# Optimization experiments

Hardware: AMD Instinct MI355X
Metric: run time of the kernel (lower is better)

The kernel has to match this reference:

```python
import jax, jax.numpy as jnp
import numpy as np


def setup_inputs() -> dict:
    key = jax.random.key(0)
    ks = jax.random.split(key, 13)
    B, T, F = 4096, 512, 64
    P, M = 64, 64  # price / metrics embedding dims
    TD, ED = 1, 8  # target_dim, explanatory_dim
    s = 0.05
    return {
        "input_seq": jax.random.normal(ks[0], (B, T, F), jnp.float32),
        "m_Wih": jax.random.normal(ks[1], (M, F + P), jnp.float32) * s,
        "m_Whh": jax.random.normal(ks[2], (M, M), jnp.float32) * s,
        "m_bih": jax.random.normal(ks[3], (M,), jnp.float32) * s,
        "m_bhh": jax.random.normal(ks[4], (M,), jnp.float32) * s,
        "p_Wih": jax.random.normal(ks[5], (P, F + M), jnp.float32) * s,
        "p_Whh": jax.random.normal(ks[6], (P, P), jnp.float32) * s,
        "p_bih": jax.random.normal(ks[7], (P,), jnp.float32) * s,
        "p_bhh": jax.random.normal(ks[8], (P,), jnp.float32) * s,
        "price_lin_W": jax.random.normal(ks[9], (TD, P), jnp.float32) * s,
        "price_lin_b": jax.random.normal(ks[10], (TD,), jnp.float32) * s,
        "metrics_lin_W": jax.random.normal(ks[11], (ED, M), jnp.float32) * s,
        "metrics_lin_b": jax.random.normal(ks[12], (ED,), jnp.float32) * s,
    }


def reference(input_seq, m_Wih, m_Whh, m_bih, m_bhh,
              p_Wih, p_Whh, p_bih, p_bhh,
              price_lin_W, price_lin_b, metrics_lin_W, metrics_lin_b):
    B = input_seq.shape[0]
    P = p_Whh.shape[0]
    M = m_Whh.shape[0]
    p0 = jnp.zeros((B, P), input_seq.dtype)
    m0 = jnp.zeros((B, M), input_seq.dtype)

    def step(carry, x_t):  # x_t: [B, F]
        p, m = carry
        # metrics cell: input = cat(x_t, price_embedding)
        m = jnp.tanh(jnp.concatenate([x_t, p], axis=1) @ m_Wih.T + m_bih
                     + m @ m_Whh.T + m_bhh)
        # price cell: input = cat(x_t, metrics_embedding)
        p = jnp.tanh(jnp.concatenate([x_t, m], axis=1) @ p_Wih.T + p_bih
                     + p @ p_Whh.T + p_bhh)
        return (p, m), None

    (p, m), _ = jax.lax.scan(step, (p0, m0), jnp.swapaxes(input_seq, 0, 1))
    # dropout in eval mode = identity
    price_pred = p @ price_lin_W.T + price_lin_b
    metrics_pred = m @ metrics_lin_W.T + metrics_lin_b
    return (price_pred, metrics_pred)
```

## Files before the change

kernel.cpp:

```cpp
#include <hip/hip_runtime.h>

typedef short bf16x8 __attribute__((ext_vector_type(8)));
typedef float f32x4 __attribute__((ext_vector_type(4)));
typedef int   int4v  __attribute__((ext_vector_type(4)));

#define MFMA16(a, b, c) __builtin_amdgcn_mfma_f32_16x16x32_bf16((a), (b), (c), 0, 0, 0)

static constexpr int T_LEN = 512;
static constexpr int F_DIM = 64;
static constexpr int NB    = 8;
static constexpr float C1  = 2.885390081777927f;

__device__ __forceinline__ unsigned short brne(float f) {
  unsigned u = __float_as_uint(f);
  return (unsigned short)((u + 0x7fffu + ((u >> 16) & 1u)) >> 16);
}

__device__ __forceinline__ int cvtpk(float lo, float hi) {
  int r;
  asm("v_cvt_pk_bf16_f32 %0, %1, %2" : "=v"(r) : "v"(lo), "v"(hi));
  return r;
}

__device__ __forceinline__ bf16x8 cvt8(const float4 &a, const float4 &b) {
  int4v d = {cvtpk(a.x, a.y), cvtpk(a.z, a.w), cvtpk(b.x, b.y), cvtpk(b.z, b.w)};
  union { int4v i; bf16x8 h; } u;
  u.i = d;
  return u.h;
}

__device__ __forceinline__ void swap32(float &a, float &b) {
  auto r = __builtin_amdgcn_permlane32_swap(__float_as_int(a), __float_as_int(b),
                                            false, false);
  a = __int_as_float(r[0]);
  b = __int_as_float(r[1]);
}

__device__ __forceinline__ float xor1(float v) {
  return __int_as_float(__builtin_amdgcn_mov_dpp(__float_as_int(v), 0xB1, 0xF, 0xF, true));
}

__device__ __forceinline__ float tanh_fold(float s, float c2) {
  float e  = __builtin_amdgcn_exp2f(__builtin_fmaf(s, C1, c2));
  float rc = __builtin_amdgcn_rcpf(e + 1.0f);
  return __builtin_fmaf(-2.0f, rc, 1.0f);
}

template<int PAR, bool FIN>
__device__ __forceinline__ void epilogue(
    const f32x4 &a0, const f32x4 &a1, float c2,
    unsigned short (*buf)[72], float (*fin)[68],
    int wofs, bool evn, int rowA, int j)
{
  float z0 = a0[0] + a1[0];
  float z1 = a0[1] + a1[1];
  float z2 = a0[2] + a1[2];
  float z3 = a0[3] + a1[3];
  swap32(z0, z2);
  swap32(z1, z3);
  float sA = (PAR == 0) ? z0 : z2;
  float sB = (PAR == 0) ? z1 : z3;
  float tA = tanh_fold(sA, c2);
  float tB = tanh_fold(sB, c2);
  float nA = xor1(tA);
  float nB = xor1(tB);
  if (evn) {
    unsigned short *p = &buf[0][0];
    *(unsigned *)(p + wofs)      = (unsigned)cvtpk(tA, nA);
    *(unsigned *)(p + wofs + 72) = (unsigned)cvtpk(tB, nB);
  }
  if (FIN) {
    fin[rowA][j]     = tA;
    fin[rowA + 1][j] = tB;
  }
}

template<int PAR, bool FIN>
__device__ __forceinline__ void step_cells(
    int arow, int g8, int j, int wofs, bool evn, int rowA,
    const bf16x8 &x0, const bf16x8 &x1,
    const bf16x8 (&Bm)[6], const bf16x8 (&Bp)[6],
    float c2m, float c2p, const f32x4 &Z,
    unsigned short (*sm_c)[72], unsigned short (*sm_p)[72],
    unsigned short (*sp_c)[72], unsigned short (*sp_p)[72],
    float (*mfin)[68], float (*pfin)[68])
{
  bf16x8 p0 = *(const bf16x8 *)&sp_p[arow][g8];
  bf16x8 p1 = *(const bf16x8 *)&sp_p[arow][32 + g8];

  {
    bf16x8 m0 = *(const bf16x8 *)&sm_p[arow][g8];
    bf16x8 m1 = *(const bf16x8 *)&sm_p[arow][32 + g8];
    f32x4 a0 = MFMA16(x0, Bm[0], Z);
    f32x4 a1 = MFMA16(x1, Bm[1], Z);
    a0 = MFMA16(p0, Bm[2], a0);
    a1 = MFMA16(p1, Bm[3], a1);
    a0 = MFMA16(m0, Bm[4], a0);
    a1 = MFMA16(m1, Bm[5], a1);
    epilogue<PAR, FIN>(a0, a1, c2m, sm_c, mfin, wofs, evn, rowA, j);
  }
  __syncthreads();
  {
    bf16x8 n0 = *(const bf16x8 *)&sm_c[arow][g8];
    bf16x8 n1 = *(const bf16x8 *)&sm_c[arow][32 + g8];
    f32x4 a0 = MFMA16(x0, Bp[0], Z);
    f32x4 a1 = MFMA16(x1, Bp[1], Z);
    a0 = MFMA16(n0, Bp[2], a0);
    a1 = MFMA16(n1, Bp[3], a1);
    a0 = MFMA16(p0, Bp[4], a0);
    a1 = MFMA16(p1, Bp[5], a1);
    epilogue<PAR, FIN>(a0, a1, c2p, sp_c, pfin, wofs, evn, rowA, j);
  }
  __syncthreads();
}

__global__ __launch_bounds__(256, 2)
void mr_rnn_kernel(const float *__restrict__ x,
                   const float *__restrict__ mWih, const float *__restrict__ mWhh,
                   const float *__restrict__ mbih, const float *__restrict__ mbhh,
                   const float *__restrict__ pWih, const float *__restrict__ pWhh,
                   const float *__restrict__ pbih, const float *__restrict__ pbhh,
                   const float *__restrict__ plW,  const float *__restrict__ plb,
                   const float *__restrict__ mlW,  const float *__restrict__ mlb,
                   float *__restrict__ out, int B)
{
  __shared__ __align__(16) unsigned short sm[2][NB][72], sp[2][NB][72];
  __shared__ __align__(16) float s_mfin[NB][68], s_pfin[NB][68];

  const int tid  = threadIdx.x;
  const int lane = tid & 63;
  const int q    = tid >> 6;
  const int l15  = lane & 15;
  const int arow = l15 & (NB - 1);
  const int half = l15 >> 3;
  const int g    = lane >> 4;
  const int j    = q * 16 + l15;
  const int b0   = blockIdx.x * NB;
  const int g8   = g * 8;
  const int rowA = ((lane & 16) >> 2) | ((lane >> 5) << 1);
  const bool evn = (l15 & 1) == 0;
  const int wofs = rowA * 72 + (j & ~1);

  bf16x8 Bm[6], Bp[6];
#pragma unroll
  for (int kt = 0; kt < 6; ++kt) {
    const int k0 = kt * 32 + g8;
#pragma unroll
    for (int i = 0; i < 8; ++i) {
      const int k = k0 + i;
      float wm = (k < 128) ? mWih[j * 128 + k] : mWhh[j * 64 + (k - 128)];
      float wp = (k < 128) ? pWih[j * 128 + k] : pWhh[j * 64 + (k - 128)];
      Bm[kt][i] = (short)brne(wm);
      Bp[kt][i] = (short)brne(wp);
    }
  }
  const float c2m = C1 * (mbih[j] + mbhh[j]);
  const float c2p = C1 * (pbih[j] + pbhh[j]);
  const f32x4 Z = {0.f, 0.f, 0.f, 0.f};

  for (int idx = tid; idx < NB * 72; idx += 256) {
    const int bb = idx / 72, kk = idx % 72;
    sm[1][bb][kk] = 0;
    sp[1][bb][kk] = 0;
  }

  const float *pxl = x + ((size_t)(b0 + arow) * T_LEN + half) * F_DIM + g8;
  float4 A0 = *(const float4 *)(pxl);
  float4 A1 = *(const float4 *)(pxl + 4);
  float4 A2 = *(const float4 *)(pxl + 32);
  float4 A3 = *(const float4 *)(pxl + 36);
  bf16x8 x0 = cvt8(A0, A1);
  bf16x8 x1 = cvt8(A2, A3);
  __syncthreads();

#pragma unroll 1
  for (int t = 0; t < T_LEN - 2; t += 2) {
    pxl += 2 * F_DIM;
    A0 = *(const float4 *)(pxl);
    A1 = *(const float4 *)(pxl + 4);
    A2 = *(const float4 *)(pxl + 32);
    A3 = *(const float4 *)(pxl + 36);
    step_cells<0, false>(arow, g8, j, wofs, evn, rowA, x0, x1, Bm, Bp, c2m, c2p, Z,
                         sm[0], sm[1], sp[0], sp[1], s_mfin, s_pfin);
    step_cells<1, false>(arow, g8, j, wofs, evn, rowA, x0, x1, Bm, Bp, c2m, c2p, Z,
                         sm[1], sm[0], sp[1], sp[0], s_mfin, s_pfin);
    x0 = cvt8(A0, A1);
    x1 = cvt8(A2, A3);
  }
  step_cells<0, false>(arow, g8, j, wofs, evn, rowA, x0, x1, Bm, Bp, c2m, c2p, Z,
                       sm[0], sm[1], sp[0], sp[1], s_mfin, s_pfin);
  step_cells<1, true>(arow, g8, j, wofs, evn, rowA, x0, x1, Bm, Bp, c2m, c2p, Z,
                      sm[1], sm[0], sp[1], sp[0], s_mfin, s_pfin);

  if (tid < NB) {
    const int b = tid;
    float acc = plb[0];
#pragma unroll 1
    for (int k = 0; k < 64; ++k) acc += s_pfin[b][k] * plW[k];
    out[b0 + b] = acc;
  } else if (tid < NB + NB * 8) {
    const int r = tid - NB;
    const int b = r >> 3, e = r & 7;
    float acc = mlb[e];
#pragma unroll 1
    for (int k = 0; k < 64; ++k) acc += s_mfin[b][k] * mlW[e * 64 + k];
    out[(size_t)B + (size_t)(b0 + b) * 8 + e] = acc;
  }
}

extern "C" void kernel_launch(void* const* d_in, const int* in_sizes, int n_in,
                              void* d_out, int out_size, void* d_ws, size_t ws_size,
                              hipStream_t stream) {
  (void)n_in; (void)out_size; (void)d_ws; (void)ws_size;
  const float* x    = (const float*)d_in[0];
  const float* mWih = (const float*)d_in[1];
  const float* mWhh = (const float*)d_in[2];
  const float* mbih = (const float*)d_in[3];
  const float* mbhh = (const float*)d_in[4];
  const float* pWih = (const float*)d_in[5];
  const float* pWhh = (const float*)d_in[6];
  const float* pbih = (const float*)d_in[7];
  const float* pbhh = (const float*)d_in[8];
  const float* plW  = (const float*)d_in[9];
  const float* plb  = (const float*)d_in[10];
  const float* mlW  = (const float*)d_in[11];
  const float* mlb  = (const float*)d_in[12];
  const int B = in_sizes[0] / (T_LEN * F_DIM);
  const int nblk = B / NB;
  mr_rnn_kernel<<<dim3(nblk), dim3(256), 0, stream>>>(
      x, mWih, mWhh, mbih, mbhh, pWih, pWhh, pbih, pbhh,
      plW, plb, mlW, mlb, (float*)d_out, B);
}
```

Baseline: 287.0 us.

## Halve batch per block to 4 rows and use 2 waves each owning 32 outputs

Each block now handles 4 batch rows with 128 threads (2 waves) instead of 8 rows with 4 waves. Each wave computes two 16-column output tiles with interleaved MFMA chains, and the result redistribution uses permlane16/permlane32 swaps. The goal is twice as many blocks for better CU coverage and cheaper barriers with fewer waves. In exchange each wave holds twice the weight registers and does twice the MFMA work per step, which lengthens the serial per-step latency.

```diff
diff --git a/kernel.cpp b/kernel.cpp
--- a/kernel.cpp
+++ b/kernel.cpp
@@ -2,13 +2,12 @@
 
 typedef short bf16x8 __attribute__((ext_vector_type(8)));
 typedef float f32x4 __attribute__((ext_vector_type(4)));
-typedef int   int4v  __attribute__((ext_vector_type(4)));
 
 #define MFMA16(a, b, c) __builtin_amdgcn_mfma_f32_16x16x32_bf16((a), (b), (c), 0, 0, 0)
 
 static constexpr int T_LEN = 512;
 static constexpr int F_DIM = 64;
-static constexpr int NB    = 8;
+static constexpr int NB    = 4;
 static constexpr float C1  = 2.885390081777927f;
 
 __device__ __forceinline__ unsigned short brne(float f) {
@@ -23,19 +22,13 @@
 }
 
 __device__ __forceinline__ bf16x8 cvt8(const float4 &a, const float4 &b) {
+  typedef int int4v __attribute__((ext_vector_type(4)));
   int4v d = {cvtpk(a.x, a.y), cvtpk(a.z, a.w), cvtpk(b.x, b.y), cvtpk(b.z, b.w)};
   union { int4v i; bf16x8 h; } u;
   u.i = d;
   return u.h;
 }
 
-__device__ __forceinline__ void swap32(float &a, float &b) {
-  auto r = __builtin_amdgcn_permlane32_swap(__float_as_int(a), __float_as_int(b),
-                                            false, false);
-  a = __int_as_float(r[0]);
-  b = __int_as_float(r[1]);
-}
-
 __device__ __forceinline__ float xor1(float v) {
   return __int_as_float(__builtin_amdgcn_mov_dpp(__float_as_int(v), 0xB1, 0xF, 0xF, true));
 }
@@ -46,41 +39,26 @@
   return __builtin_fmaf(-2.0f, rc, 1.0f);
 }
 
-template<int PAR, bool FIN>
-__device__ __forceinline__ void epilogue(
-    const f32x4 &a0, const f32x4 &a1, float c2,
-    unsigned short (*buf)[72], float (*fin)[68],
-    int wofs, bool evn, int rowA, int j)
-{
-  float z0 = a0[0] + a1[0];
-  float z1 = a0[1] + a1[1];
-  float z2 = a0[2] + a1[2];
-  float z3 = a0[3] + a1[3];
-  swap32(z0, z2);
-  swap32(z1, z3);
-  float sA = (PAR == 0) ? z0 : z2;
-  float sB = (PAR == 0) ? z1 : z3;
-  float tA = tanh_fold(sA, c2);
-  float tB = tanh_fold(sB, c2);
-  float nA = xor1(tA);
-  float nB = xor1(tB);
-  if (evn) {
-    unsigned short *p = &buf[0][0];
-    *(unsigned *)(p + wofs)      = (unsigned)cvtpk(tA, nA);
-    *(unsigned *)(p + wofs + 72) = (unsigned)cvtpk(tB, nB);
-  }
-  if (FIN) {
-    fin[rowA][j]     = tA;
-    fin[rowA + 1][j] = tB;
-  }
+template<int PAR>
+__device__ __forceinline__ float redist(const f32x4 &a0, const f32x4 &a1) {
+  int z0 = __float_as_int(a0[0] + a1[0]);
+  int z1 = __float_as_int(a0[1] + a1[1]);
+  int z2 = __float_as_int(a0[2] + a1[2]);
+  int z3 = __float_as_int(a0[3] + a1[3]);
+  auto r01 = __builtin_amdgcn_permlane16_swap(z0, z1, false, false);
+  auto r23 = __builtin_amdgcn_permlane16_swap(z2, z3, false, false);
+  int lo = (PAR == 0) ? r01[0] : r01[1];
+  int hi = (PAR == 0) ? r23[0] : r23[1];
+  auto f = __builtin_amdgcn_permlane32_swap(lo, hi, false, false);
+  return __int_as_float(f[0]);
 }
 
 template<int PAR, bool FIN>
 __device__ __forceinline__ void step_cells(
-    int arow, int g8, int j, int wofs, bool evn, int rowA,
+    int arow, int g8, int wofsA, int rowF, int jA, bool evn,
     const bf16x8 &x0, const bf16x8 &x1,
-    const bf16x8 (&Bm)[6], const bf16x8 (&Bp)[6],
-    float c2m, float c2p, const f32x4 &Z,
+    const bf16x8 (&Bm)[2][6], const bf16x8 (&Bp)[2][6],
+    const float (&c2m)[2], const float (&c2p)[2], const f32x4 &Z,
     unsigned short (*sm_c)[72], unsigned short (*sm_p)[72],
     unsigned short (*sp_c)[72], unsigned short (*sp_p)[72],
     float (*mfin)[68], float (*pfin)[68])
@@ -91,30 +69,60 @@
   {
     bf16x8 m0 = *(const bf16x8 *)&sm_p[arow][g8];
     bf16x8 m1 = *(const bf16x8 *)&sm_p[arow][32 + g8];
-    f32x4 a0 = MFMA16(x0, Bm[0], Z);
-    f32x4 a1 = MFMA16(x1, Bm[1], Z);
-    a0 = MFMA16(p0, Bm[2], a0);
-    a1 = MFMA16(p1, Bm[3], a1);
-    a0 = MFMA16(m0, Bm[4], a0);
-    a1 = MFMA16(m1, Bm[5], a1);
-    epilogue<PAR, FIN>(a0, a1, c2m, sm_c, mfin, wofs, evn, rowA, j);
+    f32x4 a00 = MFMA16(x0, Bm[0][0], Z);
+    f32x4 a01 = MFMA16(x1, Bm[0][1], Z);
+    f32x4 a10 = MFMA16(x0, Bm[1][0], Z);
+    f32x4 a11 = MFMA16(x1, Bm[1][1], Z);
+    a00 = MFMA16(p0, Bm[0][2], a00);
+    a01 = MFMA16(p1, Bm[0][3], a01);
+    a10 = MFMA16(p0, Bm[1][2], a10);
+    a11 = MFMA16(p1, Bm[1][3], a11);
+    a00 = MFMA16(m0, Bm[0][4], a00);
+    a01 = MFMA16(m1, Bm[0][5], a01);
+    a10 = MFMA16(m0, Bm[1][4], a10);
+    a11 = MFMA16(m1, Bm[1][5], a11);
+    float tA = tanh_fold(redist<PAR>(a00, a01), c2m[0]);
+    float tB = tanh_fold(redist<PAR>(a10, a11), c2m[1]);
+    float nA = xor1(tA);
+    float nB = xor1(tB);
+    if (evn) {
+      unsigned short *p = &sm_c[0][0];
+      *(unsigned *)(p + wofsA)      = (unsigned)cvtpk(tA, nA);
+      *(unsigned *)(p + wofsA + 16) = (unsigned)cvtpk(tB, nB);
+    }
+    if (FIN) { mfin[rowF][jA] = tA; mfin[rowF][jA + 16] = tB; }
   }
   __syncthreads();
   {
     bf16x8 n0 = *(const bf16x8 *)&sm_c[arow][g8];
     bf16x8 n1 = *(const bf16x8 *)&sm_c[arow][32 + g8];
-    f32x4 a0 = MFMA16(x0, Bp[0], Z);
-    f32x4 a1 = MFMA16(x1, Bp[1], Z);
-    a0 = MFMA16(n0, Bp[2], a0);
-    a1 = MFMA16(n1, Bp[3], a1);
-    a0 = MFMA16(p0, Bp[4], a0);
-    a1 = MFMA16(p1, Bp[5], a1);
-    epilogue<PAR, FIN>(a0, a1, c2p, sp_c, pfin, wofs, evn, rowA, j);
+    f32x4 a00 = MFMA16(x0, Bp[0][0], Z);
+    f32x4 a01 = MFMA16(x1, Bp[0][1], Z);
+    f32x4 a10 = MFMA16(x0, Bp[1][0], Z);
+    f32x4 a11 = MFMA16(x1, Bp[1][1], Z);
+    a00 = MFMA16(p0, Bp[0][4], a00);
+    a01 = MFMA16(p1, Bp[0][5], a01);
+    a10 = MFMA16(p0, Bp[1][4], a10);
+    a11 = MFMA16(p1, Bp[1][5], a11);
+    a00 = MFMA16(n0, Bp[0][2], a00);
+    a01 = MFMA16(n1, Bp[0][3], a01);
+    a10 = MFMA16(n0, Bp[1][2], a10);
+    a11 = MFMA16(n1, Bp[1][3], a11);
+    float tA = tanh_fold(redist<PAR>(a00, a01), c2p[0]);
+    float tB = tanh_fold(redist<PAR>(a10, a11), c2p[1]);
+    float nA = xor1(tA);
+    float nB = xor1(tB);
+    if (evn) {
+      unsigned short *p = &sp_c[0][0];
+      *(unsigned *)(p + wofsA)      = (unsigned)cvtpk(tA, nA);
+      *(unsigned *)(p + wofsA + 16) = (unsigned)cvtpk(tB, nB);
+    }
+    if (FIN) { pfin[rowF][jA] = tA; pfin[rowF][jA + 16] = tB; }
   }
   __syncthreads();
 }
 
-__global__ __launch_bounds__(256, 2)
+__global__ __launch_bounds__(128, 2)
 void mr_rnn_kernel(const float *__restrict__ x,
                    const float *__restrict__ mWih, const float *__restrict__ mWhh,
                    const float *__restrict__ mbih, const float *__restrict__ mbhh,
@@ -129,36 +137,40 @@
 
   const int tid  = threadIdx.x;
   const int lane = tid & 63;
-  const int q    = tid >> 6;
+  const int w    = tid >> 6;
   const int l15  = lane & 15;
   const int arow = l15 & (NB - 1);
-  const int half = l15 >> 3;
-  const int g    = lane >> 4;
-  const int j    = q * 16 + l15;
+  const int half = (l15 >> 2) & 1;
+  const int g8   = (lane >> 4) * 8;
+  const int rowF = lane >> 4;
   const int b0   = blockIdx.x * NB;
-  const int g8   = g * 8;
-  const int rowA = ((lane & 16) >> 2) | ((lane >> 5) << 1);
+  const int jA   = w * 32 + l15;
   const bool evn = (l15 & 1) == 0;
-  const int wofs = rowA * 72 + (j & ~1);
-
-  bf16x8 Bm[6], Bp[6];
+  const int wofsA = rowF * 72 + w * 32 + (l15 & ~1);
+
+  bf16x8 Bm[2][6], Bp[2][6];
+  float c2m[2], c2p[2];
 #pragma unroll
-  for (int kt = 0; kt < 6; ++kt) {
-    const int k0 = kt * 32 + g8;
+  for (int ct = 0; ct < 2; ++ct) {
+    const int j = w * 32 + ct * 16 + l15;
 #pragma unroll
-    for (int i = 0; i < 8; ++i) {
-      const int k = k0 + i;
-      float wm = (k < 128) ? mWih[j * 128 + k] : mWhh[j * 64 + (k - 128)];
-      float wp = (k < 128) ? pWih[j * 128 + k] : pWhh[j * 64 + (k - 128)];
-      Bm[kt][i] = (short)brne(wm);
-      Bp[kt][i] = (short)brne(wp);
+    for (int kt = 0; kt < 6; ++kt) {
+      const int k0 = kt * 32 + g8;
+#pragma unroll
+      for (int i = 0; i < 8; ++i) {
+        const int k = k0 + i;
+        float wm = (k < 128) ? mWih[j * 128 + k] : mWhh[j * 64 + (k - 128)];
+        float wp = (k < 128) ? pWih[j * 128 + k] : pWhh[j * 64 + (k - 128)];
+        Bm[ct][kt][i] = (short)brne(wm);
+        Bp[ct][kt][i] = (short)brne(wp);
+      }
     }
-  }
-  const float c2m = C1 * (mbih[j] + mbhh[j]);
-  const float c2p = C1 * (pbih[j] + pbhh[j]);
+    c2m[ct] = C1 * (mbih[j] + mbhh[j]);
+    c2p[ct] = C1 * (pbih[j] + pbhh[j]);
+  }
   const f32x4 Z = {0.f, 0.f, 0.f, 0.f};
 
-  for (int idx = tid; idx < NB * 72; idx += 256) {
+  for (int idx = tid; idx < NB * 72; idx += 128) {
     const int bb = idx / 72, kk = idx % 72;
     sm[1][bb][kk] = 0;
     sp[1][bb][kk] = 0;
@@ -180,16 +192,20 @@
     A1 = *(const float4 *)(pxl + 4);
     A2 = *(const float4 *)(pxl + 32);
     A3 = *(const float4 *)(pxl + 36);
-    step_cells<0, false>(arow, g8, j, wofs, evn, rowA, x0, x1, Bm, Bp, c2m, c2p, Z,
+    step_cells<0, false>(arow, g8, wofsA, rowF, jA, evn, x0, x1, Bm, Bp,
+                         c2m, c2p, Z,
                          sm[0], sm[1], sp[0], sp[1], s_mfin, s_pfin);
-    step_cells<1, false>(arow, g8, j, wofs, evn, rowA, x0, x1, Bm, Bp, c2m, c2p, Z,
+    step_cells<1, false>(arow, g8, wofsA, rowF, jA, evn, x0, x1, Bm, Bp,
+                         c2m, c2p, Z,
                          sm[1], sm[0], sp[1], sp[0], s_mfin, s_pfin);
     x0 = cvt8(A0, A1);
     x1 = cvt8(A2, A3);
   }
-  step_cells<0, false>(arow, g8, j, wofs, evn, rowA, x0, x1, Bm, Bp, c2m, c2p, Z,
+  step_cells<0, false>(arow, g8, wofsA, rowF, jA, evn, x0, x1, Bm, Bp,
+                       c2m, c2p, Z,
                        sm[0], sm[1], sp[0], sp[1], s_mfin, s_pfin);
-  step_cells<1, true>(arow, g8, j, wofs, evn, rowA, x0, x1, Bm, Bp, c2m, c2p, Z,
+  step_cells<1, true>(arow, g8, wofsA, rowF, jA, evn, x0, x1, Bm, Bp,
+                      c2m, c2p, Z,
                       sm[1], sm[0], sp[1], sp[0], s_mfin, s_pfin);
 
   if (tid < NB) {
@@ -227,7 +243,7 @@
   const float* mlb  = (const float*)d_in[12];
   const int B = in_sizes[0] / (T_LEN * F_DIM);
   const int nblk = B / NB;
-  mr_rnn_kernel<<<dim3(nblk), dim3(256), 0, stream>>>(
+  mr_rnn_kernel<<<dim3(nblk), dim3(128), 0, stream>>>(
       x, mWih, mWhh, mbih, mbhh, pWih, pWhh, pbih, pbhh,
       plW, plb, mlW, mlb, (float*)d_out, B);
 }
```

After: 358.8 us. +25.0%, slower.
